# Performance work log

Measured on AMD Instinct MI355X. Metric: run time of the kernel, lower is better.

Reference implementation:

```python
import jax, jax.numpy as jnp
import numpy as np

N = 50000      # num nodes
E = 800000     # num edges
IN = 512       # in_feats (= num_hidden)
H = 8          # num_heads
D = 64         # out_feats per head (H*D = 512)
NEG_SLOPE = 0.2


def setup_inputs() -> dict:
    key = jax.random.key(0)
    ks = jax.random.split(key, 7)
    feat = jax.random.normal(ks[0], (N, IN), jnp.float32)
    src = jax.random.randint(ks[1], (E,), 0, N)
    dst = jax.random.randint(ks[2], (E,), 0, N)
    W_fc = jax.random.normal(ks[3], (IN, H * D), jnp.float32) * (1.0 / np.sqrt(IN))
    W_res = jax.random.normal(ks[4], (IN, H * D), jnp.float32) * (1.0 / np.sqrt(IN))
    attn_l = jax.random.normal(ks[5], (1, H, D), jnp.float32) * 0.1
    attn_r = jax.random.normal(ks[6], (1, H, D), jnp.float32) * 0.1
    return {"feat": feat, "src": src, "dst": dst, "W_fc": W_fc,
            "W_res": W_res, "attn_l": attn_l, "attn_r": attn_r}


def reference(feat, src, dst, W_fc, W_res, attn_l, attn_r):
    # fc: [N, IN] @ [IN, H*D] -> [N, H, D]
    ft = (feat @ W_fc).reshape(N, H, D)
    # attention logits per node: el = sum(ft * attn_l, -1), er likewise -> [N, H]
    el = jnp.sum(ft * attn_l, axis=-1)
    er = jnp.sum(ft * attn_r, axis=-1)
    # u_add_v on edges, then LeakyReLU -> [E, H]
    e = jax.nn.leaky_relu(el[src] + er[dst], negative_slope=NEG_SLOPE)
    # edge_softmax: normalize over incoming edges of each dst node
    m = jax.ops.segment_max(e, dst, num_segments=N)            # [N, H]
    m = jnp.where(jnp.isfinite(m), m, jnp.zeros_like(m))       # guard zero-in-degree
    ex = jnp.exp(e - m[dst])                                   # [E, H]
    s = jax.ops.segment_sum(ex, dst, num_segments=N)           # [N, H]
    a = ex / jnp.maximum(s[dst], 1e-9)                         # [E, H]
    # u_mul_e + sum aggregation: gather src features, weight, scatter-add to dst
    msg = ft[src] * a[:, :, None]                              # [E, H, D]
    rst = jax.ops.segment_sum(msg, dst, num_segments=N)        # [N, H, D]
    # residual: res_fc Linear since in_dst_feats != out_feats
    rst = rst + (feat @ W_res).reshape(N, H, D)
    return rst
```

## Files before the change

kernel.cpp:

```cpp
#include <hip/hip_runtime.h>
#include <hip/hip_bf16.h>

#define NN 50000
#define EE 800000
#define INF 512
#define HH 8
#define DD 64
#define HD 512
#define NTOT 1024

typedef unsigned short u16;
typedef u16 u16x8 __attribute__((ext_vector_type(8)));
typedef __bf16 bf16x8 __attribute__((ext_vector_type(8)));
typedef float f32x4 __attribute__((ext_vector_type(4)));

__device__ __forceinline__ float bf2f(u16 u) {
    return __uint_as_float(((unsigned)u) << 16);
}
__device__ __forceinline__ u16 f2bf(float f) {
    __hip_bfloat16 h = __float2bfloat16(f);
    return *reinterpret_cast<u16*>(&h);
}

__global__ __launch_bounds__(256) void sniff5_kernel(const u16* __restrict__ p0,
                                                     const u16* __restrict__ p1,
                                                     const u16* __restrict__ p2,
                                                     const u16* __restrict__ p3,
                                                     const u16* __restrict__ p4,
                                                     int* __restrict__ flags) {
    const u16* ps[5] = {p0, p1, p2, p3, p4};
    const u16* p = ps[blockIdx.x];
    __shared__ int bad;
    if (threadIdx.x == 0) bad = 0;
    __syncthreads();
    float v = fabsf(bf2f(p[2 * threadIdx.x]));
    if (!(v < 1e4f)) atomicAdd(&bad, 1);
    __syncthreads();
    if (threadIdx.x == 0) flags[blockIdx.x] = (bad >= 8) ? 1 : 0;
}

__global__ __launch_bounds__(256) void transpose_kernel(const void* __restrict__ in,
                                                        u16* __restrict__ out,
                                                        const int* __restrict__ flag) {
    __shared__ u16 tile[64][65];
    const int isf32 = *flag;
    int tr = (blockIdx.x & 7) * 64;
    int tc = (blockIdx.x >> 3) * 64;
    for (int idx = threadIdx.x; idx < 64 * 64; idx += 256) {
        int r = idx >> 6, c = idx & 63;
        int g = (tr + r) * 512 + tc + c;
        tile[r][c] = isf32 ? f2bf(((const float*)in)[g]) : ((const u16*)in)[g];
    }
    __syncthreads();
    for (int idx = threadIdx.x; idx < 64 * 64; idx += 256) {
        int r = idx >> 6, c = idx & 63;
        out[(tc + r) * 512 + tr + c] = tile[c][r];
    }
}

__global__ void zero_deg_kernel(int* __restrict__ deg) {
    int t = blockIdx.x * 256 + threadIdx.x;
    if (t < NN) deg[t] = 0;
}

__global__ void count_kernel(const int* __restrict__ dst, int* __restrict__ deg) {
    int e = blockIdx.x * 256 + threadIdx.x;
    if (e < EE) atomicAdd(&deg[dst[e]], 1);
}

#define SCAN_CH 49
__global__ __launch_bounds__(1024) void scan_kernel(const int* __restrict__ deg,
                                                    int* __restrict__ rowptr,
                                                    int* __restrict__ cursor) {
    __shared__ int sums[1024];
    int t = threadIdx.x;
    int base = t * SCAN_CH;
    int s = 0;
    for (int k = 0; k < SCAN_CH; ++k) {
        int i = base + k;
        if (i < NN) s += deg[i];
    }
    sums[t] = s;
    __syncthreads();
    for (int off = 1; off < 1024; off <<= 1) {
        int v = (t >= off) ? sums[t - off] : 0;
        __syncthreads();
        sums[t] += v;
        __syncthreads();
    }
    int run = (t == 0) ? 0 : sums[t - 1];
    for (int k = 0; k < SCAN_CH; ++k) {
        int i = base + k;
        if (i < NN) {
            rowptr[i] = run;
            cursor[i] = run;
            run += deg[i];
        }
    }
    if (t == 0) rowptr[NN] = EE;
}

__global__ void scatter_kernel(const int* __restrict__ src, const int* __restrict__ dst,
                               int* __restrict__ cursor, int* __restrict__ csr_src) {
    int e = blockIdx.x * 256 + threadIdx.x;
    if (e < EE) {
        int p = atomicAdd(&cursor[dst[e]], 1);
        csr_src[p] = src[e];
    }
}

#define TM 128
#define TN 128
#define BK 32
#define LDK 40

__global__ __launch_bounds__(256) void gemm_kernel(const void* __restrict__ A,
                                                   const u16* __restrict__ Wt,
                                                   u16* __restrict__ ft,
                                                   float* __restrict__ outf,
                                                   const int* __restrict__ flag) {
    __shared__ u16 As[TM * LDK];
    __shared__ u16 Bs[TN * LDK];
    const int isf32 = *flag;
    const int bid = blockIdx.x;
    const int m0 = (bid >> 3) * TM;
    const int n0 = (bid & 7) * TN;
    const int tid = threadIdx.x;
    const int lane = tid & 63;
    const int wave = tid >> 6;
    const int wr = (wave >> 1) * 64;
    const int wc = (wave & 1) * 64;
    const int lrow = lane & 15;
    const int quad = lane >> 4;

    f32x4 acc[4][4] = {};

    for (int k0 = 0; k0 < INF; k0 += BK) {
        __syncthreads();
#pragma unroll
        for (int it = 0; it < 2; ++it) {
            int chunk = tid + it * 256;
            int r = chunk >> 2;
            int c = (chunk & 3) * 8;
            int gr = m0 + r;
            u16x8 av = {0, 0, 0, 0, 0, 0, 0, 0};
            if (gr < NN) {
                if (isf32) {
                    const f32x4* ap = (const f32x4*)((const float*)A + gr * INF + k0 + c);
                    f32x4 f0 = ap[0], f1 = ap[1];
#pragma unroll
                    for (int j = 0; j < 4; ++j) { av[j] = f2bf(f0[j]); av[4 + j] = f2bf(f1[j]); }
                } else {
                    av = *(const u16x8*)((const u16*)A + gr * INF + k0 + c);
                }
            }
            *(u16x8*)(As + r * LDK + c) = av;
            *(u16x8*)(Bs + r * LDK + c) = *(const u16x8*)(Wt + (n0 + r) * INF + k0 + c);
        }
        __syncthreads();

        bf16x8 af[4], bfr[4];
#pragma unroll
        for (int mi = 0; mi < 4; ++mi)
            af[mi] = *(const bf16x8*)(As + (wr + mi * 16 + lrow) * LDK + quad * 8);
#pragma unroll
        for (int ni = 0; ni < 4; ++ni)
            bfr[ni] = *(const bf16x8*)(Bs + (wc + ni * 16 + lrow) * LDK + quad * 8);
#pragma unroll
        for (int mi = 0; mi < 4; ++mi)
#pragma unroll
            for (int ni = 0; ni < 4; ++ni)
                acc[mi][ni] = __builtin_amdgcn_mfma_f32_16x16x32_bf16(af[mi], bfr[ni],
                                                                      acc[mi][ni], 0, 0, 0);
    }

#pragma unroll
    for (int mi = 0; mi < 4; ++mi) {
        int rb = m0 + wr + mi * 16 + quad * 4;
#pragma unroll
        for (int ni = 0; ni < 4; ++ni) {
            int col = n0 + wc + ni * 16 + lrow;
#pragma unroll
            for (int r = 0; r < 4; ++r) {
                int row = rb + r;
                if (row < NN) {
                    float v = acc[mi][ni][r];
                    if (col < HD) ft[row * HD + col] = f2bf(v);
                    else outf[row * HD + (col - HD)] = v;
                }
            }
        }
    }
}

__global__ __launch_bounds__(256) void attn_dot_kernel(const u16* __restrict__ ft,
                                                       const void* __restrict__ al,
                                                       const void* __restrict__ ar,
                                                       float* __restrict__ el,
                                                       float* __restrict__ er,
                                                       const int* __restrict__ flags) {
    int node = blockIdx.x * 4 + (threadIdx.x >> 6);
    if (node >= NN) return;
    int lane = threadIdx.x & 63;
    int off = lane * 8;

    float wl[8], wr_[8];
    if (flags[3]) {
        f32x4 a0 = *(const f32x4*)((const float*)al + off);
        f32x4 a1 = *(const f32x4*)((const float*)al + off + 4);
#pragma unroll
        for (int j = 0; j < 4; ++j) { wl[j] = a0[j]; wl[4 + j] = a1[j]; }
    } else {
        u16x8 a = *(const u16x8*)((const u16*)al + off);
#pragma unroll
        for (int j = 0; j < 8; ++j) wl[j] = bf2f(a[j]);
    }
    if (flags[4]) {
        f32x4 a0 = *(const f32x4*)((const float*)ar + off);
        f32x4 a1 = *(const f32x4*)((const float*)ar + off + 4);
#pragma unroll
        for (int j = 0; j < 4; ++j) { wr_[j] = a0[j]; wr_[4 + j] = a1[j]; }
    } else {
        u16x8 a = *(const u16x8*)((const u16*)ar + off);
#pragma unroll
        for (int j = 0; j < 8; ++j) wr_[j] = bf2f(a[j]);
    }

    u16x8 f = *(const u16x8*)(ft + node * HD + off);
    float vl = 0.0f, vr = 0.0f;
#pragma unroll
    for (int j = 0; j < 8; ++j) {
        float x = bf2f(f[j]);
        vl += x * wl[j];
        vr += x * wr_[j];
    }
#pragma unroll
    for (int msk = 1; msk < 8; msk <<= 1) {
        vl += __shfl_xor(vl, msk);
        vr += __shfl_xor(vr, msk);
    }
    if ((lane & 7) == 0) {
        el[node * HH + (lane >> 3)] = vl;
        er[node * HH + (lane >> 3)] = vr;
    }
}

__global__ __launch_bounds__(256) void aggregate_kernel(const int* __restrict__ rowptr,
                                                        const int* __restrict__ csr_src,
                                                        const u16* __restrict__ ft,
                                                        const float* __restrict__ el,
                                                        const float* __restrict__ er,
                                                        float* __restrict__ outf) {
    int node = blockIdx.x * 4 + (threadIdx.x >> 6);
    if (node >= NN) return;
    int lane = threadIdx.x & 63;
    int head = lane >> 3;
    int beg = rowptr[node], end = rowptr[node + 1];
    float erd = er[node * HH + head];

    float m = -INFINITY;
    float sden = 0.0f;
    float acc[8] = {};

    float el_n = 0.0f;
    u16x8 f_n = {};
    if (beg < end) {
        int s0 = csr_src[beg];
        el_n = el[s0 * HH + head];
        f_n = *(const u16x8*)(ft + s0 * HD + lane * 8);
    }
    for (int i = beg; i < end; ++i) {
        float elv = el_n;
        u16x8 f = f_n;
        if (i + 1 < end) {
            int s2 = csr_src[i + 1];
            el_n = el[s2 * HH + head];
            f_n = *(const u16x8*)(ft + s2 * HD + lane * 8);
        }
        float v = elv + erd;
        v = v > 0.0f ? v : 0.2f * v;
        float nm = fmaxf(m, v);
        float scale = __expf(m - nm);
        float ex = __expf(v - nm);
        m = nm;
        sden = sden * scale + ex;
#pragma unroll
        for (int j = 0; j < 8; ++j) acc[j] = acc[j] * scale + bf2f(f[j]) * ex;
    }

    float inv = 1.0f / fmaxf(sden, 1e-9f);
    float* op = outf + node * HD + lane * 8;
    f32x4 r0 = *(const f32x4*)op;
    f32x4 r1 = *(const f32x4*)(op + 4);
    f32x4 o0, o1;
#pragma unroll
    for (int j = 0; j < 4; ++j) {
        o0[j] = acc[j] * inv + r0[j];
        o1[j] = acc[4 + j] * inv + r1[j];
    }
    *(f32x4*)op = o0;
    *(f32x4*)(op + 4) = o1;
}

extern "C" void kernel_launch(void* const* d_in, const int* in_sizes, int n_in,
                              void* d_out, int out_size, void* d_ws, size_t ws_size,
                              hipStream_t stream) {
    const void* feat   = d_in[0];
    const int*  src    = (const int*)d_in[1];
    const int*  dst    = (const int*)d_in[2];
    const void* W_fc   = d_in[3];
    const void* W_res  = d_in[4];
    const void* attn_l = d_in[5];
    const void* attn_r = d_in[6];
    float* outf = (float*)d_out;

    char* ws = (char*)d_ws;
    int*   flags   = (int*)(ws);
    u16*   Wt      = (u16*)(ws + 256);
    u16*   ft      = (u16*)(ws + 1048832);
    float* el      = (float*)(ws + 52248832);
    float* er      = (float*)(ws + 53848832);
    int*   deg     = (int*)(ws + 55448832);
    int*   rowptr  = (int*)(ws + 55648832);
    int*   cursor  = (int*)(ws + 55848896);
    int*   csr_src = (int*)(ws + 56048896);

    sniff5_kernel<<<5, 256, 0, stream>>>((const u16*)feat, (const u16*)W_fc,
                                         (const u16*)W_res, (const u16*)attn_l,
                                         (const u16*)attn_r, flags);
    transpose_kernel<<<64, 256, 0, stream>>>(W_fc, Wt, flags + 1);
    transpose_kernel<<<64, 256, 0, stream>>>(W_res, Wt + 512 * 512, flags + 2);

    zero_deg_kernel<<<(NN + 255) / 256, 256, 0, stream>>>(deg);
    count_kernel<<<(EE + 255) / 256, 256, 0, stream>>>(dst, deg);
    scan_kernel<<<1, 1024, 0, stream>>>(deg, rowptr, cursor);
    scatter_kernel<<<(EE + 255) / 256, 256, 0, stream>>>(src, dst, cursor, csr_src);

    int nmblk = (NN + TM - 1) / TM;
    gemm_kernel<<<nmblk * 8, 256, 0, stream>>>(feat, Wt, ft, outf, flags + 0);

    attn_dot_kernel<<<(NN + 3) / 4, 256, 0, stream>>>(ft, attn_l, attn_r, el, er, flags);
    aggregate_kernel<<<(NN + 3) / 4, 256, 0, stream>>>(rowptr, csr_src, ft, el, er, outf);
}
```

Before: 720.5 us.

## Load GEMM tiles directly to LDS with swizzle, BK=64, grouped block order

The GEMM now uses global_load_lds to copy A and W tiles straight into shared memory, skipping the register round-trip. Tiles use an XOR-swizzled layout in place of padding to avoid bank conflicts. fp32 activations are now stored raw in LDS and converted to bf16 at fragment read time. BK doubles to 64, and block indices are remapped so eight consecutive blocks share N-tiles for L2 reuse. LDS use grows (48KB), which may reduce occupancy, and edge rows are clamped instead of zero-filled.

```diff
diff --git a/kernel.cpp b/kernel.cpp
--- a/kernel.cpp
+++ b/kernel.cpp
@@ -20,6 +20,12 @@
 __device__ __forceinline__ u16 f2bf(float f) {
     __hip_bfloat16 h = __float2bfloat16(f);
     return *reinterpret_cast<u16*>(&h);
+}
+
+__device__ __forceinline__ void gload_lds16(const void* g, void* l) {
+    __builtin_amdgcn_global_load_lds(
+        (const __attribute__((address_space(1))) void*)g,
+        (__attribute__((address_space(3))) void*)l, 16, 0, 0);
 }
 
 __global__ __launch_bounds__(256) void sniff5_kernel(const u16* __restrict__ p0,
@@ -111,20 +117,25 @@
 
 #define TM 128
 #define TN 128
-#define BK 32
-#define LDK 40
+#define BK 64
+#define NMBLK 392
 
 __global__ __launch_bounds__(256) void gemm_kernel(const void* __restrict__ A,
                                                    const u16* __restrict__ Wt,
                                                    u16* __restrict__ ft,
                                                    float* __restrict__ outf,
                                                    const int* __restrict__ flag) {
-    __shared__ u16 As[TM * LDK];
-    __shared__ u16 Bs[TN * LDK];
+    __shared__ char smem[TM * BK * 4 + TN * BK * 2];
+    float* Asf = (float*)smem;
+    u16*   As16 = (u16*)smem;
+    u16*   Bs = (u16*)(smem + TM * BK * 4);
+
     const int isf32 = *flag;
     const int bid = blockIdx.x;
-    const int m0 = (bid >> 3) * TM;
-    const int n0 = (bid & 7) * TN;
+    const int r8 = bid & 7;
+    const int q = bid >> 3;
+    const int m0 = (((q >> 3) << 3) | r8) * TM;
+    const int n0 = (q & 7) * TN;
     const int tid = threadIdx.x;
     const int lane = tid & 63;
     const int wave = tid >> 6;
@@ -137,41 +148,86 @@
 
     for (int k0 = 0; k0 < INF; k0 += BK) {
         __syncthreads();
-#pragma unroll
-        for (int it = 0; it < 2; ++it) {
-            int chunk = tid + it * 256;
-            int r = chunk >> 2;
-            int c = (chunk & 3) * 8;
-            int gr = m0 + r;
-            u16x8 av = {0, 0, 0, 0, 0, 0, 0, 0};
-            if (gr < NN) {
-                if (isf32) {
-                    const f32x4* ap = (const f32x4*)((const float*)A + gr * INF + k0 + c);
-                    f32x4 f0 = ap[0], f1 = ap[1];
-#pragma unroll
-                    for (int j = 0; j < 4; ++j) { av[j] = f2bf(f0[j]); av[4 + j] = f2bf(f1[j]); }
-                } else {
-                    av = *(const u16x8*)((const u16*)A + gr * INF + k0 + c);
+        if (isf32) {
+            const float* Af = (const float*)A;
+            int rg = lane >> 4;
+            int ch = (lane & 15) >> 1;
+            int hf = lane & 1;
+#pragma unroll
+            for (int g = 0; g < 8; ++g) {
+                int G = wave * 8 + g;
+                int r = G * 4 + rg;
+                int cs = ch ^ (r & 7);
+                int gr = m0 + r; gr = gr < NN ? gr : NN - 1;
+                gload_lds16(Af + (size_t)gr * INF + k0 + cs * 8 + hf * 4,
+                            Asf + G * 256);
+            }
+        } else {
+            const u16* Ab = (const u16*)A;
+            int rg = lane >> 3;
+            int ch = lane & 7;
+#pragma unroll
+            for (int g = 0; g < 4; ++g) {
+                int G = wave * 4 + g;
+                int r = G * 8 + rg;
+                int cs = ch ^ (r & 7);
+                int gr = m0 + r; gr = gr < NN ? gr : NN - 1;
+                gload_lds16(Ab + (size_t)gr * INF + k0 + cs * 8,
+                            As16 + G * 512);
+            }
+        }
+        {
+            int rg = lane >> 3;
+            int ch = lane & 7;
+#pragma unroll
+            for (int g = 0; g < 4; ++g) {
+                int G = wave * 4 + g;
+                int r = G * 8 + rg;
+                int cs = ch ^ (r & 7);
+                gload_lds16(Wt + (size_t)(n0 + r) * INF + k0 + cs * 8,
+                            Bs + G * 512);
+            }
+        }
+        __syncthreads();
+
+#pragma unroll
+        for (int ks = 0; ks < 2; ++ks) {
+            bf16x8 af[4], bfr[4];
+            if (isf32) {
+#pragma unroll
+                for (int mi = 0; mi < 4; ++mi) {
+                    int ar = wr + mi * 16 + lrow;
+                    int sc = (ks * 4 + quad) ^ (ar & 7);
+                    const f32x4* p = (const f32x4*)(Asf + ar * 64 + sc * 8);
+                    f32x4 lo = p[0], hi = p[1];
+                    u16x8 t;
+#pragma unroll
+                    for (int j = 0; j < 4; ++j) { t[j] = f2bf(lo[j]); t[4 + j] = f2bf(hi[j]); }
+                    af[mi] = *(bf16x8*)&t;
                 }
-            }
-            *(u16x8*)(As + r * LDK + c) = av;
-            *(u16x8*)(Bs + r * LDK + c) = *(const u16x8*)(Wt + (n0 + r) * INF + k0 + c);
-        }
-        __syncthreads();
-
-        bf16x8 af[4], bfr[4];
-#pragma unroll
-        for (int mi = 0; mi < 4; ++mi)
-            af[mi] = *(const bf16x8*)(As + (wr + mi * 16 + lrow) * LDK + quad * 8);
-#pragma unroll
-        for (int ni = 0; ni < 4; ++ni)
-            bfr[ni] = *(const bf16x8*)(Bs + (wc + ni * 16 + lrow) * LDK + quad * 8);
-#pragma unroll
-        for (int mi = 0; mi < 4; ++mi)
-#pragma unroll
-            for (int ni = 0; ni < 4; ++ni)
-                acc[mi][ni] = __builtin_amdgcn_mfma_f32_16x16x32_bf16(af[mi], bfr[ni],
-                                                                      acc[mi][ni], 0, 0, 0);
+            } else {
+#pragma unroll
+                for (int mi = 0; mi < 4; ++mi) {
+                    int ar = wr + mi * 16 + lrow;
+                    int sc = (ks * 4 + quad) ^ (ar & 7);
+                    u16x8 t = *(const u16x8*)(As16 + ar * 64 + sc * 8);
+                    af[mi] = *(bf16x8*)&t;
+                }
+            }
+#pragma unroll
+            for (int ni = 0; ni < 4; ++ni) {
+                int br = wc + ni * 16 + lrow;
+                int sc = (ks * 4 + quad) ^ (br & 7);
+                u16x8 t = *(const u16x8*)(Bs + br * 64 + sc * 8);
+                bfr[ni] = *(bf16x8*)&t;
+            }
+#pragma unroll
+            for (int mi = 0; mi < 4; ++mi)
+#pragma unroll
+                for (int ni = 0; ni < 4; ++ni)
+                    acc[mi][ni] = __builtin_amdgcn_mfma_f32_16x16x32_bf16(af[mi], bfr[ni],
+                                                                          acc[mi][ni], 0, 0, 0);
+        }
     }
 
 #pragma unroll
@@ -336,8 +392,7 @@
     scan_kernel<<<1, 1024, 0, stream>>>(deg, rowptr, cursor);
     scatter_kernel<<<(EE + 255) / 256, 256, 0, stream>>>(src, dst, cursor, csr_src);
 
-    int nmblk = (NN + TM - 1) / TM;
-    gemm_kernel<<<nmblk * 8, 256, 0, stream>>>(feat, Wt, ft, outf, flags + 0);
+    gemm_kernel<<<NMBLK * 8, 256, 0, stream>>>(feat, Wt, ft, outf, flags + 0);
 
     attn_dot_kernel<<<(NN + 3) / 4, 256, 0, stream>>>(ft, attn_l, attn_r, el, er, flags);
     aggregate_kernel<<<(NN + 3) / 4, 256, 0, stream>>>(rowptr, csr_src, ft, el, er, outf);
```

After: 672.9 us. 1.07x faster.
